# Optimization experiments

Measured on AMD Instinct MI355X. Metric: run time of the kernel, lower is better.

The kernel has to match this reference:

```python
import jax, jax.numpy as jnp
import numpy as np
from jax import lax

S, B, T, H, V = 128, 32, 64, 512, 32000
H2 = 2 * H


def setup_inputs() -> dict:
    key = jax.random.key(0)
    ks = jax.random.split(key, 12)
    sc = 0.02  # small init scale to keep softmax/log numerically tame
    return {
        "h_s": jax.random.normal(ks[0], (S, B, H2), jnp.float32),
        "s_mask": jnp.ones((S, B, 1), jnp.float32),
        "w_a": jax.random.normal(ks[1], (H2, H), jnp.float32) * sc,
        "v_a": jax.random.normal(ks[2], (H, H), jnp.float32) * sc,
        "u_a": jax.random.normal(ks[3], (H, 1), jnp.float32) * sc,
        "w_b": jax.random.normal(ks[4], (H, V), jnp.float32) * sc,
        "v_b": jax.random.normal(ks[5], (H2, V), jnp.float32) * sc,
        "W_ih": jax.random.normal(ks[6], (4 * H, H2), jnp.float32) * sc,
        "W_hh": jax.random.normal(ks[7], (4 * H, H), jnp.float32) * sc,
        "b_ih": jnp.zeros((4 * H,), jnp.float32),
        "b_hh": jnp.zeros((4 * H,), jnp.float32),
        "t_mask": jnp.ones((T, B), jnp.float32),
        "t_indices": jax.random.randint(ks[8], (T, B), 0, V, jnp.int32),
    }


def reference(h_s, s_mask, w_a, v_a, u_a, w_b, v_b, W_ih, W_hh, b_ih, b_hh, t_mask, t_indices):
    # h_s: [S,B,2H] encoder states, s_mask: [S,B,1]
    wa_h = h_s @ w_a  # precompute w_a(h_i) once (same math as per-step recompute): [S,B,H]
    b = b_ih + b_hh
    Tn = t_indices.shape[0]

    def step(carry, _):
        s, c = carry  # s = LSTM hidden state, c = cell state, each [B,H]
        # Bahdanau additive attention (original multiplies logits by mask, then softmax)
        scores = jnp.tanh(wa_h + s @ v_a) @ u_a          # [S,B,1]
        alpha = jax.nn.softmax(scores * s_mask, axis=0)   # [S,B,1]
        ct = jnp.sum(alpha * h_s, axis=0)                 # [B,2H]
        # torch LSTMCell: gates order i,f,g,o
        gates = ct @ W_ih.T + s @ W_hh.T + b              # [B,4H]
        i, f, g, o = jnp.split(gates, 4, axis=1)
        c_new = jax.nn.sigmoid(f) * c + jax.nn.sigmoid(i) * jnp.tanh(g)
        s_new = jax.nn.sigmoid(o) * jnp.tanh(c_new)
        p = jax.nn.softmax(s_new @ w_b + ct @ v_b, axis=1)  # [B,V]
        return (s_new, c_new), p

    nb = h_s.shape[1]
    init = (jnp.zeros((nb, H), h_s.dtype), jnp.zeros((nb, H), h_s.dtype))
    _, p_gen = lax.scan(step, init, None, length=Tn)      # [T,B,V]

    # masked mean NLL per batch element
    probs = jnp.take_along_axis(p_gen, t_indices[:, :, None], axis=2)[..., 0]  # [T,B]
    nll = -jnp.log(probs) * t_mask
    loss = jnp.sum(nll, axis=0) / jnp.sum(t_mask, axis=0)  # [B]
    return loss, p_gen
```

## Files before the change

### kernel.cpp

```cpp
#include <hip/hip_runtime.h>

typedef __attribute__((ext_vector_type(8))) short bf16x8;
typedef __attribute__((ext_vector_type(4))) float f32x4;
typedef __attribute__((ext_vector_type(4))) unsigned int u32x4;

#define NWG_ 256

__device__ __forceinline__ unsigned short f2b(float x){
  union { float f; unsigned u; } v; v.f = x;
  unsigned r = v.u + 0x7FFFu + ((v.u >> 16) & 1u);
  return (unsigned short)(r >> 16);
}
__device__ __forceinline__ float b2f(unsigned short h){
  union { float f; unsigned u; } v; v.u = ((unsigned)h) << 16; return v.f;
}
__device__ __forceinline__ float rcpf_(float x){ return __builtin_amdgcn_rcpf(x); }
__device__ __forceinline__ float tanhf_(float x){
  x = fminf(15.f, fmaxf(-15.f, x));
  float e = __expf(2.f*x);
  return (e - 1.f) * rcpf_(e + 1.f);
}
__device__ __forceinline__ float sigf_(float x){
  x = fminf(30.f, fmaxf(-30.f, x));
  return rcpf_(1.f + __expf(-x));
}

__global__ void k_convert(const float* __restrict__ h_s, const float* __restrict__ w_a,
                          const float* __restrict__ W_ih, const float* __restrict__ v_a,
                          const float* __restrict__ W_hh, const float* __restrict__ b_ih,
                          const float* __restrict__ b_hh,
                          unsigned short* __restrict__ hs_b, unsigned short* __restrict__ Wcomb,
                          unsigned short* __restrict__ Wv, unsigned short* __restrict__ Whh_p,
                          float* __restrict__ bias_p)
{
  const int total = 4194304 + 524288 + 2097152 + 262144 + 1048576 + 2048;
  for (int i = blockIdx.x*256 + threadIdx.x; i < total; i += gridDim.x*256) {
    int j = i;
    if (j < 4194304) { hs_b[j] = f2b(h_s[j]); continue; }
    j -= 4194304;
    if (j < 524288) { int k = j >> 9, n = j & 511;
      Wcomb[n*1024 + k] = f2b(w_a[k*512 + n]); continue; }
    j -= 524288;
    if (j < 2097152) { int rp = j >> 10, k = j & 1023;
      int h = rp >> 2, g = rp & 3;
      Wcomb[(512 + rp)*1024 + k] = f2b(W_ih[(g*512 + h)*1024 + k]); continue; }
    j -= 2097152;
    if (j < 262144) { int k = j >> 9, h = j & 511;
      Wv[h*512 + k] = f2b(v_a[k*512 + h]); continue; }
    j -= 262144;
    if (j < 1048576) { int rp = j >> 9, k = j & 511;
      int h = rp >> 2, g = rp & 3;
      Whh_p[rp*512 + k] = f2b(W_hh[(g*512 + h)*512 + k]); continue; }
    j -= 1048576;
    { int rp = j; int h = rp >> 2, g = rp & 3;
      bias_p[rp] = b_ih[g*512 + h] + b_hh[g*512 + h]; }
  }
}

__global__ __launch_bounds__(256) void k_convB(const float* __restrict__ w_b,
                                               const float* __restrict__ v_b,
                                               unsigned short* __restrict__ Bt)
{
  __shared__ unsigned short T[64*80];
  const int k0 = blockIdx.x*64, n0 = blockIdx.y*64;
  const int tx = threadIdx.x;
  const int kk = tx >> 4, nn = (tx & 15)*4;
  #pragma unroll
  for (int i = 0; i < 4; ++i) {
    int kr = k0 + kk + i*16;
    const float* src = (kr < 512) ? &w_b[(size_t)kr*32000 + n0 + nn]
                                  : &v_b[(size_t)(kr-512)*32000 + n0 + nn];
    f32x4 v = *(const f32x4*)src;
    T[(nn+0)*80 + kk + i*16] = f2b(v.x);
    T[(nn+1)*80 + kk + i*16] = f2b(v.y);
    T[(nn+2)*80 + kk + i*16] = f2b(v.z);
    T[(nn+3)*80 + kk + i*16] = f2b(v.w);
  }
  __syncthreads();
  #pragma unroll
  for (int i = 0; i < 2; ++i) {
    int p = tx + i*256;
    int nrow = p >> 3, kp = p & 7;
    *(u32x4*)&Bt[(size_t)(n0+nrow)*1536 + k0 + kp*8] = *(const u32x4*)&T[nrow*80 + kp*8];
  }
}

#define BM 128
#define BN 128
#define BK 64
#define LDT 72

__global__ __launch_bounds__(256) void k_gemm(
  const unsigned short* __restrict__ A,
  const float* __restrict__ B0, const float* __restrict__ B1, int bsplit,
  const unsigned short* __restrict__ Bnk, int mode,
  void* __restrict__ C0, void* __restrict__ C1, int ncut, int ldc0, int ldc1, int cbf,
  float* __restrict__ Zp,
  int M, int N, int K)
{
  __shared__ unsigned short As[BM*LDT];
  __shared__ unsigned short Bs[BN*LDT];
  const int tx = threadIdx.x;
  const int m0 = blockIdx.x * BM, n0 = blockIdx.y * BN;
  const int wave = tx >> 6, lane = tx & 63;
  const int wm = (wave >> 1) * 64, wn = (wave & 1) * 64;
  const int q = lane >> 4, r16 = lane & 15;
  f32x4 acc[4][4];
  #pragma unroll
  for (int i=0;i<4;i++)
    #pragma unroll
    for (int j=0;j<4;j++) acc[i][j] = (f32x4){0.f,0.f,0.f,0.f};

  for (int k0 = 0; k0 < K; k0 += BK) {
    #pragma unroll
    for (int i = 0; i < 4; ++i) {
      int idx = tx + i*256;
      int row = idx >> 3, piece = idx & 7;
      *(u32x4*)&As[row*LDT + piece*8] =
        *(const u32x4*)&A[(size_t)(m0+row)*K + k0 + piece*8];
    }
    if (mode == 0) {
      #pragma unroll
      for (int i = 0; i < 8; ++i) {
        int idx = tx + i*256;
        int kk = idx >> 5, nn = (idx & 31)*4;
        int kg = k0 + kk;
        const float* src = (kg < bsplit) ? (B0 + (size_t)kg*N) : (B1 + (size_t)(kg - bsplit)*N);
        f32x4 v = *(const f32x4*)&src[n0 + nn];
        Bs[(nn+0)*LDT + kk] = f2b(v.x);
        Bs[(nn+1)*LDT + kk] = f2b(v.y);
        Bs[(nn+2)*LDT + kk] = f2b(v.z);
        Bs[(nn+3)*LDT + kk] = f2b(v.w);
      }
    } else {
      #pragma unroll
      for (int i = 0; i < 4; ++i) {
        int idx = tx + i*256;
        int row = idx >> 3, piece = idx & 7;
        *(u32x4*)&Bs[row*LDT + piece*8] =
          *(const u32x4*)&Bnk[(size_t)(n0+row)*K + k0 + piece*8];
      }
    }
    __syncthreads();
    #pragma unroll
    for (int kk = 0; kk < BK; kk += 32) {
      bf16x8 af[4], bfv[4];
      #pragma unroll
      for (int i=0;i<4;i++) af[i] = *(const bf16x8*)&As[(wm + i*16 + r16)*LDT + kk + q*8];
      #pragma unroll
      for (int j=0;j<4;j++) bfv[j] = *(const bf16x8*)&Bs[(wn + j*16 + r16)*LDT + kk + q*8];
      #pragma unroll
      for (int i=0;i<4;i++)
        #pragma unroll
        for (int j=0;j<4;j++)
          acc[i][j] = __builtin_amdgcn_mfma_f32_16x16x32_bf16(af[i], bfv[j], acc[i][j], 0,0,0);
    }
    __syncthreads();
  }
  if (Zp) {
    #pragma unroll
    for (int i=0;i<4;i++)
      #pragma unroll
      for (int reg=0; reg<4; ++reg) {
        float z = __expf(acc[i][0][reg]) + __expf(acc[i][1][reg])
                + __expf(acc[i][2][reg]) + __expf(acc[i][3][reg]);
        z += __shfl_xor(z, 1, 64); z += __shfl_xor(z, 2, 64);
        z += __shfl_xor(z, 4, 64); z += __shfl_xor(z, 8, 64);
        if (r16 == 0) atomicAdd(&Zp[m0 + wm + i*16 + q*4 + reg], z);
      }
  }
  #pragma unroll
  for (int i=0;i<4;i++)
    #pragma unroll
    for (int j=0;j<4;j++) {
      int n = n0 + wn + j*16 + r16;
      #pragma unroll
      for (int reg=0; reg<4; ++reg) {
        int m = m0 + wm + i*16 + q*4 + reg;
        float v = acc[i][j][reg];
        if (n < ncut) {
          if (cbf) ((unsigned short*)C0)[(size_t)m*ldc0 + n] = f2b(v);
          else     ((float*)C0)[(size_t)m*ldc0 + n] = v;
        } else {
          if (cbf) ((unsigned short*)C1)[(size_t)m*ldc1 + (n-ncut)] = f2b(v);
          else     ((float*)C1)[(size_t)m*ldc1 + (n-ncut)] = v;
        }
      }
    }
}

__device__ __forceinline__ void gbar(unsigned* bar, int w, int* dead) {
  __syncthreads();
  if (*dead) return;
  if (threadIdx.x == 0) {
    unsigned* gen = bar + 288;
    unsigned g = __hip_atomic_load(gen, __ATOMIC_RELAXED, __HIP_MEMORY_SCOPE_AGENT);
    unsigned a = __hip_atomic_fetch_add(&bar[(w & 7)*32], 1u, __ATOMIC_ACQ_REL, __HIP_MEMORY_SCOPE_AGENT);
    bool flipped = false;
    if (a == 31u) {
      unsigned b = __hip_atomic_fetch_add(bar + 256, 1u, __ATOMIC_ACQ_REL, __HIP_MEMORY_SCOPE_AGENT);
      if (b == 7u) {
        #pragma unroll
        for (int i = 0; i < 8; ++i)
          __hip_atomic_store(&bar[i*32], 0u, __ATOMIC_RELAXED, __HIP_MEMORY_SCOPE_AGENT);
        __hip_atomic_store(bar + 256, 0u, __ATOMIC_RELAXED, __HIP_MEMORY_SCOPE_AGENT);
        __hip_atomic_store(gen, g + 1u, __ATOMIC_RELEASE, __HIP_MEMORY_SCOPE_AGENT);
        flipped = true;
      }
    }
    if (!flipped) {
      long sp = 0;
      while (__hip_atomic_load(gen, __ATOMIC_RELAXED, __HIP_MEMORY_SCOPE_AGENT) == g) {
        __builtin_amdgcn_s_sleep(8);
        if (++sp > 400000L) { *dead = 1; break; }
      }
    }
    __builtin_amdgcn_fence(__ATOMIC_ACQUIRE, "agent");
  }
  __syncthreads();
}

__global__ __launch_bounds__(256) void k_recur(
  const unsigned short* __restrict__ wa_h,
  const unsigned short* __restrict__ G,
  const unsigned short* __restrict__ hs_b,
  const unsigned short* __restrict__ Wv,
  const unsigned short* __restrict__ Whh_p,
  const float* __restrict__ bias_p,
  const float* __restrict__ s_mask,
  const float* __restrict__ u_a,
  float* __restrict__ c_st,
  float* __restrict__ sva_g,
  float* __restrict__ whh_g,
  float* __restrict__ scores_g,
  unsigned short* __restrict__ Abf,
  unsigned* bar)
{
  __shared__ float AL[128];
  __shared__ float GL[256];
  __shared__ float RD[2048];
  __shared__ int s_dead;
  const int w = blockIdx.x, tx = threadIdx.x;
  if (tx == 0) s_dead = 0;
  { int gid = w*256 + tx; if (gid < 32*512) c_st[gid] = 0.f; }
  gbar(bar, w, &s_dead);

  const int wave = tx >> 6, lane = tx & 63;
  const f32x4 ua0 = *(const f32x4*)&u_a[lane*8];
  const f32x4 ua1 = *(const f32x4*)&u_a[lane*8 + 4];

  for (int t = 0; t < 64; ++t) {
    if (w < 160) {
      if (t == 0) {
        for (int o = tx; o < 512; o += 256) {
          int b = o >> 4, rl = o & 15;
          int nc = w*16 + rl;
          if (nc < 512) sva_g[b*512 + nc] = 0.f;
          else          whh_g[b*2048 + (nc - 512)] = 0.f;
        }
      } else {
        const int q = lane >> 4, rl = lane & 15;
        const int ncol = w*16 + rl;
        const unsigned short* bp = (ncol < 512) ? (Wv + (size_t)ncol*512)
                                                : (Whh_p + (size_t)(ncol-512)*512);
        f32x4 a0 = (f32x4){0.f,0.f,0.f,0.f}, a1 = (f32x4){0.f,0.f,0.f,0.f};
        const size_t arow0 = ((size_t)(t-1)*32 + rl) * 1536;
        const size_t arow1 = ((size_t)(t-1)*32 + 16 + rl) * 1536;
        #pragma unroll
        for (int ks = 0; ks < 4; ++ks) {
          int kg = (wave*4 + ks)*32 + q*8;
          bf16x8 fa0 = *(const bf16x8*)&Abf[arow0 + kg];
          bf16x8 fa1 = *(const bf16x8*)&Abf[arow1 + kg];
          bf16x8 fb  = *(const bf16x8*)&bp[kg];
          a0 = __builtin_amdgcn_mfma_f32_16x16x32_bf16(fa0, fb, a0, 0,0,0);
          a1 = __builtin_amdgcn_mfma_f32_16x16x32_bf16(fa1, fb, a1, 0,0,0);
        }
        #pragma unroll
        for (int reg = 0; reg < 4; ++reg) {
          RD[(wave*32 + (q*4 + reg))*16 + rl]      = a0[reg];
          RD[(wave*32 + (16 + q*4 + reg))*16 + rl] = a1[reg];
        }
        __syncthreads();
        for (int o = tx; o < 512; o += 256) {
          int b = o >> 4, rlo = o & 15;
          float v = RD[(b)*16 + rlo] + RD[(32 + b)*16 + rlo]
                  + RD[(64 + b)*16 + rlo] + RD[(96 + b)*16 + rlo];
          int nc = w*16 + rlo;
          if (nc < 512) sva_g[b*512 + nc] = v;
          else          whh_g[b*2048 + (nc - 512)] = v;
        }
      }
    }
    gbar(bar, w, &s_dead);

    {
      #pragma unroll
      for (int r = 0; r < 4; ++r) {
        int p = w*16 + wave*4 + r;
        int b = p & 31, s = p >> 5;
        bf16x8 wv8 = *(const bf16x8*)&wa_h[(size_t)p*512 + lane*8];
        const float* sv = &sva_g[b*512 + lane*8];
        f32x4 s0 = *(const f32x4*)sv, s1 = *(const f32x4*)(sv + 4);
        float acc;
        acc  = tanhf_(b2f(wv8[0]) + s0.x) * ua0.x;
        acc += tanhf_(b2f(wv8[1]) + s0.y) * ua0.y;
        acc += tanhf_(b2f(wv8[2]) + s0.z) * ua0.z;
        acc += tanhf_(b2f(wv8[3]) + s0.w) * ua0.w;
        acc += tanhf_(b2f(wv8[4]) + s1.x) * ua1.x;
        acc += tanhf_(b2f(wv8[5]) + s1.y) * ua1.y;
        acc += tanhf_(b2f(wv8[6]) + s1.z) * ua1.z;
        acc += tanhf_(b2f(wv8[7]) + s1.w) * ua1.w;
        #pragma unroll
        for (int o = 32; o > 0; o >>= 1) acc += __shfl_down(acc, o, 64);
        if (lane == 0) scores_g[b*128 + s] = acc * s_mask[s*32 + b];
      }
    }
    gbar(bar, w, &s_dead);

    {
      const int b = w >> 3, ch = w & 7;
      if (tx < 128) AL[tx] = __expf(scores_g[b*128 + tx]);
      __syncthreads();
      if (tx < 64) {
        float sm = AL[tx] + AL[tx + 64];
        #pragma unroll
        for (int o = 32; o > 0; o >>= 1) sm += __shfl_down(sm, o, 64);
        if (tx == 0) GL[0] = rcpf_(sm);
      }
      __syncthreads();
      float inv = GL[0];
      __syncthreads();
      if (tx < 128) AL[tx] *= inv;
      __syncthreads();
      {
        const int cg = tx & 31, sg = tx >> 5;
        const int nn = ch*256 + cg*8;
        float a8[8] = {0.f,0.f,0.f,0.f,0.f,0.f,0.f,0.f};
        #pragma unroll
        for (int k = 0; k < 16; ++k) {
          int s = sg*16 + k;
          float av = AL[s];
          bf16x8 g8 = *(const bf16x8*)&G[((size_t)s*32 + b)*2048 + nn];
          a8[0] += av * b2f(g8[0]); a8[1] += av * b2f(g8[1]);
          a8[2] += av * b2f(g8[2]); a8[3] += av * b2f(g8[3]);
          a8[4] += av * b2f(g8[4]); a8[5] += av * b2f(g8[5]);
          a8[6] += av * b2f(g8[6]); a8[7] += av * b2f(g8[7]);
        }
        #pragma unroll
        for (int j = 0; j < 8; ++j) RD[(cg*8 + j)*8 + sg] = a8[j];
      }
      __syncthreads();
      {
        int n = ch*256 + tx;
        float sum = 0.f;
        #pragma unroll
        for (int k = 0; k < 8; ++k) sum += RD[tx*8 + k];
        GL[tx] = sum + whh_g[b*2048 + n] + bias_p[n];
      }
      __syncthreads();
      if (tx < 64) {
        int h = ch*64 + tx;
        float iv = GL[tx*4+0], fv = GL[tx*4+1], gv = GL[tx*4+2], ov = GL[tx*4+3];
        float co = c_st[b*512 + h];
        float cn = sigf_(fv)*co + sigf_(iv)*tanhf_(gv);
        float sn = sigf_(ov)*tanhf_(cn);
        c_st[b*512 + h] = cn;
        Abf[((size_t)t*32 + b)*1536 + h] = f2b(sn);
      }
      {
        const int cg2 = tx & 15, sg2 = tx >> 4;
        const int jj = ch*128 + cg2*8;
        float c8[8] = {0.f,0.f,0.f,0.f,0.f,0.f,0.f,0.f};
        #pragma unroll
        for (int k = 0; k < 8; ++k) {
          int s = sg2*8 + k;
          float av = AL[s];
          bf16x8 h8 = *(const bf16x8*)&hs_b[((size_t)s*32 + b)*1024 + jj];
          c8[0] += av * b2f(h8[0]); c8[1] += av * b2f(h8[1]);
          c8[2] += av * b2f(h8[2]); c8[3] += av * b2f(h8[3]);
          c8[4] += av * b2f(h8[4]); c8[5] += av * b2f(h8[5]);
          c8[6] += av * b2f(h8[6]); c8[7] += av * b2f(h8[7]);
        }
        __syncthreads();
        #pragma unroll
        for (int j = 0; j < 8; ++j) RD[(cg2*8 + j)*16 + sg2] = c8[j];
      }
      __syncthreads();
      if (tx < 128) {
        float sum = 0.f;
        #pragma unroll
        for (int k = 0; k < 16; ++k) sum += RD[tx*16 + k];
        Abf[((size_t)t*32 + b)*1536 + 512 + ch*128 + tx] = f2b(sum);
      }
    }
    gbar(bar, w, &s_dead);
  }
}

__global__ __launch_bounds__(64) void k_loss(const float* __restrict__ L, const float* __restrict__ Z,
                                             const int* __restrict__ t_idx, const float* __restrict__ t_mask,
                                             float* __restrict__ out)
{
  const int b = blockIdx.x, t = threadIdx.x;
  const int row = t*32 + b;
  int id = t_idx[t*32 + b];
  float m = t_mask[t*32 + b];
  float l = L[(size_t)row*32000 + id];
  float v = (__logf(Z[row]) - l) * m;
  float vm = v, mm = m;
  for (int o = 32; o > 0; o >>= 1) { vm += __shfl_down(vm, o, 64); mm += __shfl_down(mm, o, 64); }
  if (t == 0) out[b] = vm / mm;
}

__global__ __launch_bounds__(256) void k_s2(float* __restrict__ L, const float* __restrict__ Z)
{
  const int row = blockIdx.x, tx = threadIdx.x;
  float* p = L + (size_t)row*32000;
  float rz = 1.f / Z[row];
  for (int n = tx; n < 32000; n += 256) p[n] = __expf(p[n]) * rz;
}

extern "C" void kernel_launch(void* const* d_in, const int* in_sizes, int n_in,
                              void* d_out, int out_size, void* d_ws, size_t ws_size,
                              hipStream_t stream)
{
  (void)in_sizes; (void)n_in; (void)out_size;
  const float* h_s    = (const float*)d_in[0];
  const float* s_mask = (const float*)d_in[1];
  const float* w_a    = (const float*)d_in[2];
  const float* v_a    = (const float*)d_in[3];
  const float* u_a    = (const float*)d_in[4];
  const float* w_b    = (const float*)d_in[5];
  const float* v_b    = (const float*)d_in[6];
  const float* W_ih   = (const float*)d_in[7];
  const float* W_hh   = (const float*)d_in[8];
  const float* b_ih   = (const float*)d_in[9];
  const float* b_hh   = (const float*)d_in[10];
  const float* t_mask = (const float*)d_in[11];
  const int*   t_idx  = (const int*)d_in[12];
  float* out = (float*)d_out;
  float* logits = out + 32;

  char* w = (char*)d_ws;
  size_t off = 0;
  auto take = [&](size_t bytes) -> void* {
    void* p = w + off; off += (bytes + 255) & ~(size_t)255; return p;
  };
  unsigned* bar          = (unsigned*)take(2048);
  float* c_st            = (float*)take((size_t)32*512*4);
  float* sva_g           = (float*)take((size_t)32*512*4);
  float* whh_g           = (float*)take((size_t)32*2048*4);
  float* scores_g        = (float*)take((size_t)32*128*4);
  float* Z               = (float*)take((size_t)2048*4);
  float* bias_p          = (float*)take((size_t)2048*4);
  unsigned short* hs_b   = (unsigned short*)take((size_t)4096*1024*2);
  unsigned short* Wcomb  = (unsigned short*)take((size_t)2560*1024*2);
  unsigned short* Wv     = (unsigned short*)take((size_t)512*512*2);
  unsigned short* Whh_p  = (unsigned short*)take((size_t)2048*512*2);
  unsigned short* wa_hb  = (unsigned short*)take((size_t)4096*512*2);
  unsigned short* G      = (unsigned short*)take((size_t)4096*2048*2);
  unsigned short* Abf    = (unsigned short*)take((size_t)2048*1536*2);
  size_t base_need = off;
  bool useBt = (ws_size >= base_need + (size_t)32000*1536*2 + 256);
  unsigned short* Bt = useBt ? (unsigned short*)take((size_t)32000*1536*2) : nullptr;

  hipMemsetAsync(bar, 0, 2048, stream);
  hipMemsetAsync(Z, 0, 2048*4, stream);
  k_convert<<<4096, 256, 0, stream>>>(h_s, w_a, W_ih, v_a, W_hh, b_ih, b_hh,
                                      hs_b, Wcomb, Wv, Whh_p, bias_p);
  if (useBt)
    k_convB<<<dim3(24, 500), 256, 0, stream>>>(w_b, v_b, Bt);
  k_gemm<<<dim3(32,20), 256, 0, stream>>>(hs_b, nullptr, nullptr, 0, Wcomb, 1,
                                          wa_hb, G, 512, 512, 2048, 1, nullptr,
                                          4096, 2560, 1024);
  k_recur<<<NWG_, 256, 0, stream>>>(wa_hb, G, hs_b, Wv, Whh_p, bias_p, s_mask, u_a,
                                    c_st, sva_g, whh_g, scores_g, Abf, bar);
  if (useBt)
    k_gemm<<<dim3(16,250), 256, 0, stream>>>(Abf, nullptr, nullptr, 0, Bt, 1,
                                             logits, logits, 32000, 32000, 32000, 0, Z,
                                             2048, 32000, 1536);
  else
    k_gemm<<<dim3(16,250), 256, 0, stream>>>(Abf, w_b, v_b, 512, nullptr, 0,
                                             logits, logits, 32000, 32000, 32000, 0, Z,
                                             2048, 32000, 1536);
  k_loss<<<32, 64, 0, stream>>>(logits, Z, t_idx, t_mask, out);
  k_s2<<<2048, 256, 0, stream>>>(logits, Z);
}
```

Baseline: 3.015 ms.

## Replace grid-wide barriers with per-batch group barriers in recurrent kernel

The recurrent kernel now partitions work so each batch element is owned by a group of 8 workgroups, which synchronise through per-batch phase slots instead of a grid-wide 256-block barrier. The hidden-state matvecs (s@v_a and s@W_hh) are computed locally per group with scalar dot products, rather than by MFMA across 160 blocks reading Abf. Cell state and the W_hh projection are kept in shared memory, and softmax normalisation is deferred into the reductions. This cuts grid-wide synchronisation latency in exchange for more redundant weight reads per group and non-MFMA matvecs.

```diff
diff --git a/kernel.cpp b/kernel.cpp
--- a/kernel.cpp
+++ b/kernel.cpp
@@ -4,7 +4,8 @@
 typedef __attribute__((ext_vector_type(4))) float f32x4;
 typedef __attribute__((ext_vector_type(4))) unsigned int u32x4;
 
-#define NWG_ 256
+#define AG  __HIP_MEMORY_SCOPE_AGENT
+#define RLX __ATOMIC_RELAXED
 
 __device__ __forceinline__ unsigned short f2b(float x){
   union { float f; unsigned u; } v; v.f = x;
@@ -189,35 +190,34 @@
     }
 }
 
-__device__ __forceinline__ void gbar(unsigned* bar, int w, int* dead) {
+__device__ __forceinline__ void group_bar(unsigned* slots, int ch, int wv, int lane,
+                                          unsigned ph, volatile int* dead)
+{
   __syncthreads();
-  if (*dead) return;
-  if (threadIdx.x == 0) {
-    unsigned* gen = bar + 288;
-    unsigned g = __hip_atomic_load(gen, __ATOMIC_RELAXED, __HIP_MEMORY_SCOPE_AGENT);
-    unsigned a = __hip_atomic_fetch_add(&bar[(w & 7)*32], 1u, __ATOMIC_ACQ_REL, __HIP_MEMORY_SCOPE_AGENT);
-    bool flipped = false;
-    if (a == 31u) {
-      unsigned b = __hip_atomic_fetch_add(bar + 256, 1u, __ATOMIC_ACQ_REL, __HIP_MEMORY_SCOPE_AGENT);
-      if (b == 7u) {
-        #pragma unroll
-        for (int i = 0; i < 8; ++i)
-          __hip_atomic_store(&bar[i*32], 0u, __ATOMIC_RELAXED, __HIP_MEMORY_SCOPE_AGENT);
-        __hip_atomic_store(bar + 256, 0u, __ATOMIC_RELAXED, __HIP_MEMORY_SCOPE_AGENT);
-        __hip_atomic_store(gen, g + 1u, __ATOMIC_RELEASE, __HIP_MEMORY_SCOPE_AGENT);
-        flipped = true;
-      }
-    }
-    if (!flipped) {
-      long sp = 0;
-      while (__hip_atomic_load(gen, __ATOMIC_RELAXED, __HIP_MEMORY_SCOPE_AGENT) == g) {
-        __builtin_amdgcn_s_sleep(8);
-        if (++sp > 400000L) { *dead = 1; break; }
-      }
-    }
-    __builtin_amdgcn_fence(__ATOMIC_ACQUIRE, "agent");
+  if (wv == 0 && !*dead) {
+    if (lane == 0)
+      __hip_atomic_store(&slots[ch], ph, RLX, AG);
+    long sp = 0;
+    for (;;) {
+      unsigned v = __hip_atomic_load(&slots[lane & 7], RLX, AG);
+      if (__all((int)(v >= ph))) break;
+      __builtin_amdgcn_s_sleep(2);
+      if (++sp > 1500000L) { *dead = 1; break; }
+    }
   }
   __syncthreads();
+}
+
+__device__ __forceinline__ float dot8_(bf16x8 w8, const float* sp) {
+  float a0 =      b2f((unsigned short)w8[0]) * sp[0];
+  float a1 =      b2f((unsigned short)w8[1]) * sp[1];
+  a0 = fmaf(b2f((unsigned short)w8[2]), sp[2], a0);
+  a1 = fmaf(b2f((unsigned short)w8[3]), sp[3], a1);
+  a0 = fmaf(b2f((unsigned short)w8[4]), sp[4], a0);
+  a1 = fmaf(b2f((unsigned short)w8[5]), sp[5], a1);
+  a0 = fmaf(b2f((unsigned short)w8[6]), sp[6], a0);
+  a1 = fmaf(b2f((unsigned short)w8[7]), sp[7], a1);
+  return a0 + a1;
 }
 
 __global__ __launch_bounds__(256) void k_recur(
@@ -229,171 +229,164 @@
   const float* __restrict__ bias_p,
   const float* __restrict__ s_mask,
   const float* __restrict__ u_a,
-  float* __restrict__ c_st,
-  float* __restrict__ sva_g,
-  float* __restrict__ whh_g,
-  float* __restrict__ scores_g,
+  float* __restrict__ s_comm,
+  float* __restrict__ sva_comm,
+  float* __restrict__ scores_comm,
   unsigned short* __restrict__ Abf,
-  unsigned* bar)
-{
+  unsigned* __restrict__ bar)
+{
+  __shared__ float s_sh[512];
+  __shared__ float sva_sh[512];
+  __shared__ float whh_sh[256];
   __shared__ float AL[128];
   __shared__ float GL[256];
   __shared__ float RD[2048];
+  __shared__ float c_sh[64];
+  __shared__ float invs;
   __shared__ int s_dead;
+
   const int w = blockIdx.x, tx = threadIdx.x;
+  const int b = w >> 3, ch = w & 7;
+  const int wv = tx >> 6, lane = tx & 63;
+  unsigned* slots = bar + b*64;
+
   if (tx == 0) s_dead = 0;
-  { int gid = w*256 + tx; if (gid < 32*512) c_st[gid] = 0.f; }
-  gbar(bar, w, &s_dead);
-
-  const int wave = tx >> 6, lane = tx & 63;
+  if (tx < 64) c_sh[tx] = 0.f;
+  if (tx < 64)
+    __hip_atomic_store(&s_comm[b*512 + ch*64 + tx], 0.f, RLX, AG);
+
   const f32x4 ua0 = *(const f32x4*)&u_a[lane*8];
   const f32x4 ua1 = *(const f32x4*)&u_a[lane*8 + 4];
 
+  group_bar(slots, ch, wv, lane, 1u, &s_dead);
+
   for (int t = 0; t < 64; ++t) {
-    if (w < 160) {
-      if (t == 0) {
-        for (int o = tx; o < 512; o += 256) {
-          int b = o >> 4, rl = o & 15;
-          int nc = w*16 + rl;
-          if (nc < 512) sva_g[b*512 + nc] = 0.f;
-          else          whh_g[b*2048 + (nc - 512)] = 0.f;
-        }
-      } else {
-        const int q = lane >> 4, rl = lane & 15;
-        const int ncol = w*16 + rl;
-        const unsigned short* bp = (ncol < 512) ? (Wv + (size_t)ncol*512)
-                                                : (Whh_p + (size_t)(ncol-512)*512);
-        f32x4 a0 = (f32x4){0.f,0.f,0.f,0.f}, a1 = (f32x4){0.f,0.f,0.f,0.f};
-        const size_t arow0 = ((size_t)(t-1)*32 + rl) * 1536;
-        const size_t arow1 = ((size_t)(t-1)*32 + 16 + rl) * 1536;
-        #pragma unroll
-        for (int ks = 0; ks < 4; ++ks) {
-          int kg = (wave*4 + ks)*32 + q*8;
-          bf16x8 fa0 = *(const bf16x8*)&Abf[arow0 + kg];
-          bf16x8 fa1 = *(const bf16x8*)&Abf[arow1 + kg];
-          bf16x8 fb  = *(const bf16x8*)&bp[kg];
-          a0 = __builtin_amdgcn_mfma_f32_16x16x32_bf16(fa0, fb, a0, 0,0,0);
-          a1 = __builtin_amdgcn_mfma_f32_16x16x32_bf16(fa1, fb, a1, 0,0,0);
-        }
-        #pragma unroll
-        for (int reg = 0; reg < 4; ++reg) {
-          RD[(wave*32 + (q*4 + reg))*16 + rl]      = a0[reg];
-          RD[(wave*32 + (16 + q*4 + reg))*16 + rl] = a1[reg];
-        }
-        __syncthreads();
-        for (int o = tx; o < 512; o += 256) {
-          int b = o >> 4, rlo = o & 15;
-          float v = RD[(b)*16 + rlo] + RD[(32 + b)*16 + rlo]
-                  + RD[(64 + b)*16 + rlo] + RD[(96 + b)*16 + rlo];
-          int nc = w*16 + rlo;
-          if (nc < 512) sva_g[b*512 + nc] = v;
-          else          whh_g[b*2048 + (nc - 512)] = v;
-        }
-      }
-    }
-    gbar(bar, w, &s_dead);
-
+    const unsigned ph0 = 2u + 3u*(unsigned)t;
+
+    for (int i = tx; i < 512; i += 256)
+      s_sh[i] = __hip_atomic_load(&s_comm[b*512 + i], RLX, AG);
+    __syncthreads();
     {
-      #pragma unroll
-      for (int r = 0; r < 4; ++r) {
-        int p = w*16 + wave*4 + r;
-        int b = p & 31, s = p >> 5;
-        bf16x8 wv8 = *(const bf16x8*)&wa_h[(size_t)p*512 + lane*8];
-        const float* sv = &sva_g[b*512 + lane*8];
-        f32x4 s0 = *(const f32x4*)sv, s1 = *(const f32x4*)(sv + 4);
-        float acc;
-        acc  = tanhf_(b2f(wv8[0]) + s0.x) * ua0.x;
-        acc += tanhf_(b2f(wv8[1]) + s0.y) * ua0.y;
-        acc += tanhf_(b2f(wv8[2]) + s0.z) * ua0.z;
-        acc += tanhf_(b2f(wv8[3]) + s0.w) * ua0.w;
-        acc += tanhf_(b2f(wv8[4]) + s1.x) * ua1.x;
-        acc += tanhf_(b2f(wv8[5]) + s1.y) * ua1.y;
-        acc += tanhf_(b2f(wv8[6]) + s1.z) * ua1.z;
-        acc += tanhf_(b2f(wv8[7]) + s1.w) * ua1.w;
+      const float* sp = &s_sh[lane*8];
+      const unsigned short* __restrict__ wvb = Wv + (size_t)(ch*64)*512;
+      #pragma unroll 4
+      for (int r = wv; r < 64; r += 4) {
+        bf16x8 w8 = *(const bf16x8*)&wvb[(size_t)r*512 + lane*8];
+        float acc = dot8_(w8, sp);
         #pragma unroll
         for (int o = 32; o > 0; o >>= 1) acc += __shfl_down(acc, o, 64);
-        if (lane == 0) scores_g[b*128 + s] = acc * s_mask[s*32 + b];
-      }
-    }
-    gbar(bar, w, &s_dead);
-
+        if (lane == 0)
+          __hip_atomic_store(&sva_comm[b*512 + ch*64 + r], acc, RLX, AG);
+      }
+      const unsigned short* __restrict__ whb = Whh_p + (size_t)(ch*256)*512;
+      #pragma unroll 4
+      for (int r = wv; r < 256; r += 4) {
+        bf16x8 w8 = *(const bf16x8*)&whb[(size_t)r*512 + lane*8];
+        float acc = dot8_(w8, sp);
+        #pragma unroll
+        for (int o = 32; o > 0; o >>= 1) acc += __shfl_down(acc, o, 64);
+        if (lane == 0) whh_sh[r] = acc;
+      }
+    }
+    group_bar(slots, ch, wv, lane, ph0, &s_dead);
+
+    for (int i = tx; i < 512; i += 256)
+      sva_sh[i] = __hip_atomic_load(&sva_comm[b*512 + i], RLX, AG);
+    __syncthreads();
     {
-      const int b = w >> 3, ch = w & 7;
-      if (tx < 128) AL[tx] = __expf(scores_g[b*128 + tx]);
+      const float* sp = &sva_sh[lane*8];
+      #pragma unroll
+      for (int si = 0; si < 4; ++si) {
+        const int s = ch*16 + wv*4 + si;
+        bf16x8 w8 = *(const bf16x8*)&wa_h[((size_t)s*32 + b)*512 + lane*8];
+        float acc;
+        acc  = tanhf_(b2f((unsigned short)w8[0]) + sp[0]) * ua0.x;
+        acc += tanhf_(b2f((unsigned short)w8[1]) + sp[1]) * ua0.y;
+        acc += tanhf_(b2f((unsigned short)w8[2]) + sp[2]) * ua0.z;
+        acc += tanhf_(b2f((unsigned short)w8[3]) + sp[3]) * ua0.w;
+        acc += tanhf_(b2f((unsigned short)w8[4]) + sp[4]) * ua1.x;
+        acc += tanhf_(b2f((unsigned short)w8[5]) + sp[5]) * ua1.y;
+        acc += tanhf_(b2f((unsigned short)w8[6]) + sp[6]) * ua1.z;
+        acc += tanhf_(b2f((unsigned short)w8[7]) + sp[7]) * ua1.w;
+        #pragma unroll
+        for (int o = 32; o > 0; o >>= 1) acc += __shfl_down(acc, o, 64);
+        if (lane == 0)
+          __hip_atomic_store(&scores_comm[b*128 + s], acc * s_mask[s*32 + b], RLX, AG);
+      }
+    }
+    group_bar(slots, ch, wv, lane, ph0 + 1u, &s_dead);
+
+    if (tx < 128)
+      AL[tx] = __expf(__hip_atomic_load(&scores_comm[b*128 + tx], RLX, AG));
+    __syncthreads();
+    if (tx < 64) {
+      float sm = AL[tx] + AL[tx + 64];
+      #pragma unroll
+      for (int o = 32; o > 0; o >>= 1) sm += __shfl_down(sm, o, 64);
+      if (tx == 0) invs = rcpf_(sm);
+    }
+    __syncthreads();
+    {
+      const int cg = tx & 31, sg = tx >> 5;
+      const int nn = ch*256 + cg*8;
+      float a8[8] = {0.f,0.f,0.f,0.f,0.f,0.f,0.f,0.f};
+      #pragma unroll
+      for (int k = 0; k < 16; ++k) {
+        int s = sg*16 + k;
+        float av = AL[s];
+        bf16x8 g8 = *(const bf16x8*)&G[((size_t)s*32 + b)*2048 + nn];
+        a8[0] += av * b2f((unsigned short)g8[0]); a8[1] += av * b2f((unsigned short)g8[1]);
+        a8[2] += av * b2f((unsigned short)g8[2]); a8[3] += av * b2f((unsigned short)g8[3]);
+        a8[4] += av * b2f((unsigned short)g8[4]); a8[5] += av * b2f((unsigned short)g8[5]);
+        a8[6] += av * b2f((unsigned short)g8[6]); a8[7] += av * b2f((unsigned short)g8[7]);
+      }
+      #pragma unroll
+      for (int j = 0; j < 8; ++j) RD[(cg*8 + j)*8 + sg] = a8[j];
+    }
+    __syncthreads();
+    {
+      float sum = 0.f;
+      #pragma unroll
+      for (int k = 0; k < 8; ++k) sum += RD[tx*8 + k];
+      GL[tx] = sum * invs + whh_sh[tx] + bias_p[ch*256 + tx];
+    }
+    __syncthreads();
+    if (tx < 64) {
+      float iv = GL[tx*4+0], fv = GL[tx*4+1], gv = GL[tx*4+2], ov = GL[tx*4+3];
+      float co = c_sh[tx];
+      float cn = sigf_(fv)*co + sigf_(iv)*tanhf_(gv);
+      float sn = sigf_(ov)*tanhf_(cn);
+      c_sh[tx] = cn;
+      __hip_atomic_store(&s_comm[b*512 + ch*64 + tx], sn, RLX, AG);
+      Abf[((size_t)t*32 + b)*1536 + ch*64 + tx] = f2b(sn);
+    }
+    {
+      const int cg2 = tx & 15, sg2 = tx >> 4;
+      const int jj = ch*128 + cg2*8;
+      float c8[8] = {0.f,0.f,0.f,0.f,0.f,0.f,0.f,0.f};
+      #pragma unroll
+      for (int k = 0; k < 8; ++k) {
+        int s = sg2*8 + k;
+        float av = AL[s];
+        bf16x8 h8 = *(const bf16x8*)&hs_b[((size_t)s*32 + b)*1024 + jj];
+        c8[0] += av * b2f((unsigned short)h8[0]); c8[1] += av * b2f((unsigned short)h8[1]);
+        c8[2] += av * b2f((unsigned short)h8[2]); c8[3] += av * b2f((unsigned short)h8[3]);
+        c8[4] += av * b2f((unsigned short)h8[4]); c8[5] += av * b2f((unsigned short)h8[5]);
+        c8[6] += av * b2f((unsigned short)h8[6]); c8[7] += av * b2f((unsigned short)h8[7]);
+      }
       __syncthreads();
-      if (tx < 64) {
-        float sm = AL[tx] + AL[tx + 64];
-        #pragma unroll
-        for (int o = 32; o > 0; o >>= 1) sm += __shfl_down(sm, o, 64);
-        if (tx == 0) GL[0] = rcpf_(sm);
-      }
-      __syncthreads();
-      float inv = GL[0];
-      __syncthreads();
-      if (tx < 128) AL[tx] *= inv;
-      __syncthreads();
-      {
-        const int cg = tx & 31, sg = tx >> 5;
-        const int nn = ch*256 + cg*8;
-        float a8[8] = {0.f,0.f,0.f,0.f,0.f,0.f,0.f,0.f};
-        #pragma unroll
-        for (int k = 0; k < 16; ++k) {
-          int s = sg*16 + k;
-          float av = AL[s];
-          bf16x8 g8 = *(const bf16x8*)&G[((size_t)s*32 + b)*2048 + nn];
-          a8[0] += av * b2f(g8[0]); a8[1] += av * b2f(g8[1]);
-          a8[2] += av * b2f(g8[2]); a8[3] += av * b2f(g8[3]);
-          a8[4] += av * b2f(g8[4]); a8[5] += av * b2f(g8[5]);
-          a8[6] += av * b2f(g8[6]); a8[7] += av * b2f(g8[7]);
-        }
-        #pragma unroll
-        for (int j = 0; j < 8; ++j) RD[(cg*8 + j)*8 + sg] = a8[j];
-      }
-      __syncthreads();
-      {
-        int n = ch*256 + tx;
-        float sum = 0.f;
-        #pragma unroll
-        for (int k = 0; k < 8; ++k) sum += RD[tx*8 + k];
-        GL[tx] = sum + whh_g[b*2048 + n] + bias_p[n];
-      }
-      __syncthreads();
-      if (tx < 64) {
-        int h = ch*64 + tx;
-        float iv = GL[tx*4+0], fv = GL[tx*4+1], gv = GL[tx*4+2], ov = GL[tx*4+3];
-        float co = c_st[b*512 + h];
-        float cn = sigf_(fv)*co + sigf_(iv)*tanhf_(gv);
-        float sn = sigf_(ov)*tanhf_(cn);
-        c_st[b*512 + h] = cn;
-        Abf[((size_t)t*32 + b)*1536 + h] = f2b(sn);
-      }
-      {
-        const int cg2 = tx & 15, sg2 = tx >> 4;
-        const int jj = ch*128 + cg2*8;
-        float c8[8] = {0.f,0.f,0.f,0.f,0.f,0.f,0.f,0.f};
-        #pragma unroll
-        for (int k = 0; k < 8; ++k) {
-          int s = sg2*8 + k;
-          float av = AL[s];
-          bf16x8 h8 = *(const bf16x8*)&hs_b[((size_t)s*32 + b)*1024 + jj];
-          c8[0] += av * b2f(h8[0]); c8[1] += av * b2f(h8[1]);
-          c8[2] += av * b2f(h8[2]); c8[3] += av * b2f(h8[3]);
-          c8[4] += av * b2f(h8[4]); c8[5] += av * b2f(h8[5]);
-          c8[6] += av * b2f(h8[6]); c8[7] += av * b2f(h8[7]);
-        }
-        __syncthreads();
-        #pragma unroll
-        for (int j = 0; j < 8; ++j) RD[(cg2*8 + j)*16 + sg2] = c8[j];
-      }
-      __syncthreads();
-      if (tx < 128) {
-        float sum = 0.f;
-        #pragma unroll
-        for (int k = 0; k < 16; ++k) sum += RD[tx*16 + k];
-        Abf[((size_t)t*32 + b)*1536 + 512 + ch*128 + tx] = f2b(sum);
-      }
-    }
-    gbar(bar, w, &s_dead);
+      #pragma unroll
+      for (int j = 0; j < 8; ++j) RD[(cg2*8 + j)*16 + sg2] = c8[j];
+    }
+    __syncthreads();
+    if (tx < 128) {
+      float sum = 0.f;
+      #pragma unroll
+      for (int k = 0; k < 16; ++k) sum += RD[tx*16 + k];
+      Abf[((size_t)t*32 + b)*1536 + 512 + ch*128 + tx] = f2b(sum * invs);
+    }
+    if (t < 63)
+      group_bar(slots, ch, wv, lane, ph0 + 2u, &s_dead);
   }
 }
 
@@ -446,11 +439,10 @@
   auto take = [&](size_t bytes) -> void* {
     void* p = w + off; off += (bytes + 255) & ~(size_t)255; return p;
   };
-  unsigned* bar          = (unsigned*)take(2048);
-  float* c_st            = (float*)take((size_t)32*512*4);
-  float* sva_g           = (float*)take((size_t)32*512*4);
-  float* whh_g           = (float*)take((size_t)32*2048*4);
-  float* scores_g        = (float*)take((size_t)32*128*4);
+  unsigned* bar          = (unsigned*)take((size_t)32*64*4);
+  float* s_comm          = (float*)take((size_t)32*512*4);
+  float* sva_comm        = (float*)take((size_t)32*512*4);
+  float* scores_comm     = (float*)take((size_t)32*128*4);
   float* Z               = (float*)take((size_t)2048*4);
   float* bias_p          = (float*)take((size_t)2048*4);
   unsigned short* hs_b   = (unsigned short*)take((size_t)4096*1024*2);
@@ -464,7 +456,7 @@
   bool useBt = (ws_size >= base_need + (size_t)32000*1536*2 + 256);
   unsigned short* Bt = useBt ? (unsigned short*)take((size_t)32000*1536*2) : nullptr;
 
-  hipMemsetAsync(bar, 0, 2048, stream);
+  hipMemsetAsync(bar, 0, (size_t)32*64*4, stream);
   hipMemsetAsync(Z, 0, 2048*4, stream);
   k_convert<<<4096, 256, 0, stream>>>(h_s, w_a, W_ih, v_a, W_hh, b_ih, b_hh,
                                       hs_b, Wcomb, Wv, Whh_p, bias_p);
@@ -473,8 +465,8 @@
   k_gemm<<<dim3(32,20), 256, 0, stream>>>(hs_b, nullptr, nullptr, 0, Wcomb, 1,
                                           wa_hb, G, 512, 512, 2048, 1, nullptr,
                                           4096, 2560, 1024);
-  k_recur<<<NWG_, 256, 0, stream>>>(wa_hb, G, hs_b, Wv, Whh_p, bias_p, s_mask, u_a,
-                                    c_st, sva_g, whh_g, scores_g, Abf, bar);
+  k_recur<<<256, 256, 0, stream>>>(wa_hb, G, hs_b, Wv, Whh_p, bias_p, s_mask, u_a,
+                                   s_comm, sva_comm, scores_comm, Abf, bar);
   if (useBt)
     k_gemm<<<dim3(16,250), 256, 0, stream>>>(Abf, nullptr, nullptr, 0, Bt, 1,
                                              logits, logits, 32000, 32000, 32000, 0, Z,
```

After: 4.229 ms. +40.3%, slower.

## Use monotonic-phase grid barrier and keep LSTM state on-chip in recurrence

Applied to the files above, without the earlier changes.

Replaces the generation-counter grid barrier, which reset its counters every round, with a monotonic phase-counting barrier that has 16 sub-counters and uses relaxed atomics plus an explicit vmcnt wait. The initial barrier and the barrier after the final step are dropped. Cell state now lives in LDS per workgroup, and the hidden state is published as packed bf16 through a small buffer that is staged into LDS before the matvec. Cross-workgroup data is read and written with agent-scope atomics so that caches do not return stale values. This cuts barrier latency and global traffic per step, but correctness now relies on relaxed-ordering memory semantics.

```diff
diff --git a/kernel.cpp b/kernel.cpp
--- a/kernel.cpp
+++ b/kernel.cpp
@@ -4,7 +4,8 @@
 typedef __attribute__((ext_vector_type(4))) float f32x4;
 typedef __attribute__((ext_vector_type(4))) unsigned int u32x4;
 
-#define NWG_ 256
+#define AG  __HIP_MEMORY_SCOPE_AGENT
+#define RLX __ATOMIC_RELAXED
 
 __device__ __forceinline__ unsigned short f2b(float x){
   union { float f; unsigned u; } v; v.f = x;
@@ -189,33 +190,23 @@
     }
 }
 
-__device__ __forceinline__ void gbar(unsigned* bar, int w, int* dead) {
+__device__ __forceinline__ void gbar(unsigned* bar, int w, unsigned ph, volatile int* dead) {
   __syncthreads();
   if (*dead) return;
   if (threadIdx.x == 0) {
-    unsigned* gen = bar + 288;
-    unsigned g = __hip_atomic_load(gen, __ATOMIC_RELAXED, __HIP_MEMORY_SCOPE_AGENT);
-    unsigned a = __hip_atomic_fetch_add(&bar[(w & 7)*32], 1u, __ATOMIC_ACQ_REL, __HIP_MEMORY_SCOPE_AGENT);
-    bool flipped = false;
-    if (a == 31u) {
-      unsigned b = __hip_atomic_fetch_add(bar + 256, 1u, __ATOMIC_ACQ_REL, __HIP_MEMORY_SCOPE_AGENT);
-      if (b == 7u) {
-        #pragma unroll
-        for (int i = 0; i < 8; ++i)
-          __hip_atomic_store(&bar[i*32], 0u, __ATOMIC_RELAXED, __HIP_MEMORY_SCOPE_AGENT);
-        __hip_atomic_store(bar + 256, 0u, __ATOMIC_RELAXED, __HIP_MEMORY_SCOPE_AGENT);
-        __hip_atomic_store(gen, g + 1u, __ATOMIC_RELEASE, __HIP_MEMORY_SCOPE_AGENT);
-        flipped = true;
-      }
-    }
-    if (!flipped) {
-      long sp = 0;
-      while (__hip_atomic_load(gen, __ATOMIC_RELAXED, __HIP_MEMORY_SCOPE_AGENT) == g) {
-        __builtin_amdgcn_s_sleep(8);
-        if (++sp > 400000L) { *dead = 1; break; }
-      }
-    }
-    __builtin_amdgcn_fence(__ATOMIC_ACQUIRE, "agent");
+    asm volatile("s_waitcnt vmcnt(0)" ::: "memory");
+    unsigned* gen = bar + 520;
+    unsigned a = __hip_atomic_fetch_add(&bar[(w & 15)*32], 1u, RLX, AG);
+    if (a == ph*16u - 1u) {
+      unsigned m = __hip_atomic_fetch_add(bar + 512, 1u, RLX, AG);
+      if (m == ph*16u - 1u)
+        __hip_atomic_store(gen, ph, RLX, AG);
+    }
+    long sp = 0;
+    while (__hip_atomic_load(gen, RLX, AG) < ph) {
+      __builtin_amdgcn_s_sleep(4);
+      if (++sp > 3000000L) { *dead = 1; break; }
+    }
   }
   __syncthreads();
 }
@@ -229,69 +220,69 @@
   const float* __restrict__ bias_p,
   const float* __restrict__ s_mask,
   const float* __restrict__ u_a,
-  float* __restrict__ c_st,
   float* __restrict__ sva_g,
   float* __restrict__ whh_g,
   float* __restrict__ scores_g,
+  unsigned* __restrict__ s_bf,
   unsigned short* __restrict__ Abf,
   unsigned* bar)
 {
+  __shared__ unsigned s_lds[32*260];
   __shared__ float AL[128];
   __shared__ float GL[256];
   __shared__ float RD[2048];
+  __shared__ float c_sh[64];
   __shared__ int s_dead;
+
   const int w = blockIdx.x, tx = threadIdx.x;
+  const int wave = tx >> 6, lane = tx & 63;
   if (tx == 0) s_dead = 0;
-  { int gid = w*256 + tx; if (gid < 32*512) c_st[gid] = 0.f; }
-  gbar(bar, w, &s_dead);
-
-  const int wave = tx >> 6, lane = tx & 63;
+  if (tx < 64) c_sh[tx] = 0.f;
+
   const f32x4 ua0 = *(const f32x4*)&u_a[lane*8];
   const f32x4 ua1 = *(const f32x4*)&u_a[lane*8 + 4];
 
   for (int t = 0; t < 64; ++t) {
+    const unsigned ph0 = 1u + 3u*(unsigned)t;
+
     if (w < 160) {
-      if (t == 0) {
-        for (int o = tx; o < 512; o += 256) {
-          int b = o >> 4, rl = o & 15;
-          int nc = w*16 + rl;
-          if (nc < 512) sva_g[b*512 + nc] = 0.f;
-          else          whh_g[b*2048 + (nc - 512)] = 0.f;
-        }
-      } else {
-        const int q = lane >> 4, rl = lane & 15;
-        const int ncol = w*16 + rl;
-        const unsigned short* bp = (ncol < 512) ? (Wv + (size_t)ncol*512)
-                                                : (Whh_p + (size_t)(ncol-512)*512);
-        f32x4 a0 = (f32x4){0.f,0.f,0.f,0.f}, a1 = (f32x4){0.f,0.f,0.f,0.f};
-        const size_t arow0 = ((size_t)(t-1)*32 + rl) * 1536;
-        const size_t arow1 = ((size_t)(t-1)*32 + 16 + rl) * 1536;
-        #pragma unroll
-        for (int ks = 0; ks < 4; ++ks) {
-          int kg = (wave*4 + ks)*32 + q*8;
-          bf16x8 fa0 = *(const bf16x8*)&Abf[arow0 + kg];
-          bf16x8 fa1 = *(const bf16x8*)&Abf[arow1 + kg];
-          bf16x8 fb  = *(const bf16x8*)&bp[kg];
-          a0 = __builtin_amdgcn_mfma_f32_16x16x32_bf16(fa0, fb, a0, 0,0,0);
-          a1 = __builtin_amdgcn_mfma_f32_16x16x32_bf16(fa1, fb, a1, 0,0,0);
-        }
-        #pragma unroll
-        for (int reg = 0; reg < 4; ++reg) {
-          RD[(wave*32 + (q*4 + reg))*16 + rl]      = a0[reg];
-          RD[(wave*32 + (16 + q*4 + reg))*16 + rl] = a1[reg];
-        }
-        __syncthreads();
-        for (int o = tx; o < 512; o += 256) {
-          int b = o >> 4, rlo = o & 15;
-          float v = RD[(b)*16 + rlo] + RD[(32 + b)*16 + rlo]
-                  + RD[(64 + b)*16 + rlo] + RD[(96 + b)*16 + rlo];
-          int nc = w*16 + rlo;
-          if (nc < 512) sva_g[b*512 + nc] = v;
-          else          whh_g[b*2048 + (nc - 512)] = v;
-        }
-      }
-    }
-    gbar(bar, w, &s_dead);
+      #pragma unroll 8
+      for (int i = tx; i < 32*256; i += 256) {
+        unsigned v = __hip_atomic_load(&s_bf[i], RLX, AG);
+        s_lds[(i >> 8)*260 + (i & 255)] = v;
+      }
+      __syncthreads();
+      const int q = lane >> 4, rl = lane & 15;
+      const int ncol = w*16 + rl;
+      const unsigned short* bp = (ncol < 512) ? (Wv + (size_t)ncol*512)
+                                              : (Whh_p + (size_t)(ncol-512)*512);
+      f32x4 a0 = (f32x4){0.f,0.f,0.f,0.f}, a1 = (f32x4){0.f,0.f,0.f,0.f};
+      #pragma unroll
+      for (int ks = 0; ks < 4; ++ks) {
+        int kg = (wave*4 + ks)*32 + q*8;
+        int ku = (wave*4 + ks)*16 + q*4;
+        bf16x8 fa0 = *(const bf16x8*)&s_lds[rl*260 + ku];
+        bf16x8 fa1 = *(const bf16x8*)&s_lds[(16 + rl)*260 + ku];
+        bf16x8 fb  = *(const bf16x8*)&bp[kg];
+        a0 = __builtin_amdgcn_mfma_f32_16x16x32_bf16(fa0, fb, a0, 0,0,0);
+        a1 = __builtin_amdgcn_mfma_f32_16x16x32_bf16(fa1, fb, a1, 0,0,0);
+      }
+      #pragma unroll
+      for (int reg = 0; reg < 4; ++reg) {
+        RD[(wave*32 + (q*4 + reg))*16 + rl]      = a0[reg];
+        RD[(wave*32 + (16 + q*4 + reg))*16 + rl] = a1[reg];
+      }
+      __syncthreads();
+      for (int o = tx; o < 512; o += 256) {
+        int bq = o >> 4, rlo = o & 15;
+        float v = RD[bq*16 + rlo] + RD[(32 + bq)*16 + rlo]
+                + RD[(64 + bq)*16 + rlo] + RD[(96 + bq)*16 + rlo];
+        int nc = w*16 + rlo;
+        if (nc < 512) __hip_atomic_store(&sva_g[bq*512 + nc], v, RLX, AG);
+        else          __hip_atomic_store(&whh_g[bq*2048 + (nc - 512)], v, RLX, AG);
+      }
+    }
+    gbar(bar, w, ph0, &s_dead);
 
     {
       #pragma unroll
@@ -299,27 +290,31 @@
         int p = w*16 + wave*4 + r;
         int b = p & 31, s = p >> 5;
         bf16x8 wv8 = *(const bf16x8*)&wa_h[(size_t)p*512 + lane*8];
-        const float* sv = &sva_g[b*512 + lane*8];
-        f32x4 s0 = *(const f32x4*)sv, s1 = *(const f32x4*)(sv + 4);
+        float sv[8];
+        #pragma unroll
+        for (int j = 0; j < 8; ++j)
+          sv[j] = __hip_atomic_load(&sva_g[b*512 + lane*8 + j], RLX, AG);
         float acc;
-        acc  = tanhf_(b2f(wv8[0]) + s0.x) * ua0.x;
-        acc += tanhf_(b2f(wv8[1]) + s0.y) * ua0.y;
-        acc += tanhf_(b2f(wv8[2]) + s0.z) * ua0.z;
-        acc += tanhf_(b2f(wv8[3]) + s0.w) * ua0.w;
-        acc += tanhf_(b2f(wv8[4]) + s1.x) * ua1.x;
-        acc += tanhf_(b2f(wv8[5]) + s1.y) * ua1.y;
-        acc += tanhf_(b2f(wv8[6]) + s1.z) * ua1.z;
-        acc += tanhf_(b2f(wv8[7]) + s1.w) * ua1.w;
+        acc  = tanhf_(b2f((unsigned short)wv8[0]) + sv[0]) * ua0.x;
+        acc += tanhf_(b2f((unsigned short)wv8[1]) + sv[1]) * ua0.y;
+        acc += tanhf_(b2f((unsigned short)wv8[2]) + sv[2]) * ua0.z;
+        acc += tanhf_(b2f((unsigned short)wv8[3]) + sv[3]) * ua0.w;
+        acc += tanhf_(b2f((unsigned short)wv8[4]) + sv[4]) * ua1.x;
+        acc += tanhf_(b2f((unsigned short)wv8[5]) + sv[5]) * ua1.y;
+        acc += tanhf_(b2f((unsigned short)wv8[6]) + sv[6]) * ua1.z;
+        acc += tanhf_(b2f((unsigned short)wv8[7]) + sv[7]) * ua1.w;
         #pragma unroll
         for (int o = 32; o > 0; o >>= 1) acc += __shfl_down(acc, o, 64);
-        if (lane == 0) scores_g[b*128 + s] = acc * s_mask[s*32 + b];
-      }
-    }
-    gbar(bar, w, &s_dead);
+        if (lane == 0)
+          __hip_atomic_store(&scores_g[b*128 + s], acc * s_mask[s*32 + b], RLX, AG);
+      }
+    }
+    gbar(bar, w, ph0 + 1u, &s_dead);
 
     {
       const int b = w >> 3, ch = w & 7;
-      if (tx < 128) AL[tx] = __expf(scores_g[b*128 + tx]);
+      if (tx < 128)
+        AL[tx] = __expf(__hip_atomic_load(&scores_g[b*128 + tx], RLX, AG));
       __syncthreads();
       if (tx < 64) {
         float sm = AL[tx] + AL[tx + 64];
@@ -341,10 +336,10 @@
           int s = sg*16 + k;
           float av = AL[s];
           bf16x8 g8 = *(const bf16x8*)&G[((size_t)s*32 + b)*2048 + nn];
-          a8[0] += av * b2f(g8[0]); a8[1] += av * b2f(g8[1]);
-          a8[2] += av * b2f(g8[2]); a8[3] += av * b2f(g8[3]);
-          a8[4] += av * b2f(g8[4]); a8[5] += av * b2f(g8[5]);
-          a8[6] += av * b2f(g8[6]); a8[7] += av * b2f(g8[7]);
+          a8[0] += av * b2f((unsigned short)g8[0]); a8[1] += av * b2f((unsigned short)g8[1]);
+          a8[2] += av * b2f((unsigned short)g8[2]); a8[3] += av * b2f((unsigned short)g8[3]);
+          a8[4] += av * b2f((unsigned short)g8[4]); a8[5] += av * b2f((unsigned short)g8[5]);
+          a8[6] += av * b2f((unsigned short)g8[6]); a8[7] += av * b2f((unsigned short)g8[7]);
         }
         #pragma unroll
         for (int j = 0; j < 8; ++j) RD[(cg*8 + j)*8 + sg] = a8[j];
@@ -355,17 +350,23 @@
         float sum = 0.f;
         #pragma unroll
         for (int k = 0; k < 8; ++k) sum += RD[tx*8 + k];
-        GL[tx] = sum + whh_g[b*2048 + n] + bias_p[n];
+        GL[tx] = sum + __hip_atomic_load(&whh_g[b*2048 + n], RLX, AG) + bias_p[n];
       }
       __syncthreads();
       if (tx < 64) {
-        int h = ch*64 + tx;
         float iv = GL[tx*4+0], fv = GL[tx*4+1], gv = GL[tx*4+2], ov = GL[tx*4+3];
-        float co = c_st[b*512 + h];
+        float co = c_sh[tx];
         float cn = sigf_(fv)*co + sigf_(iv)*tanhf_(gv);
         float sn = sigf_(ov)*tanhf_(cn);
-        c_st[b*512 + h] = cn;
-        Abf[((size_t)t*32 + b)*1536 + h] = f2b(sn);
+        c_sh[tx] = cn;
+        int h = ch*64 + tx;
+        unsigned short hb = f2b(sn);
+        Abf[((size_t)t*32 + b)*1536 + h] = hb;
+        unsigned nb = (unsigned)__shfl_down((int)hb, 1, 64);
+        if ((tx & 1) == 0) {
+          unsigned pk = (unsigned)hb | (nb << 16);
+          __hip_atomic_store(&s_bf[b*256 + (h >> 1)], pk, RLX, AG);
+        }
       }
       {
         const int cg2 = tx & 15, sg2 = tx >> 4;
@@ -376,10 +377,10 @@
           int s = sg2*8 + k;
           float av = AL[s];
           bf16x8 h8 = *(const bf16x8*)&hs_b[((size_t)s*32 + b)*1024 + jj];
-          c8[0] += av * b2f(h8[0]); c8[1] += av * b2f(h8[1]);
-          c8[2] += av * b2f(h8[2]); c8[3] += av * b2f(h8[3]);
-          c8[4] += av * b2f(h8[4]); c8[5] += av * b2f(h8[5]);
-          c8[6] += av * b2f(h8[6]); c8[7] += av * b2f(h8[7]);
+          c8[0] += av * b2f((unsigned short)h8[0]); c8[1] += av * b2f((unsigned short)h8[1]);
+          c8[2] += av * b2f((unsigned short)h8[2]); c8[3] += av * b2f((unsigned short)h8[3]);
+          c8[4] += av * b2f((unsigned short)h8[4]); c8[5] += av * b2f((unsigned short)h8[5]);
+          c8[6] += av * b2f((unsigned short)h8[6]); c8[7] += av * b2f((unsigned short)h8[7]);
         }
         __syncthreads();
         #pragma unroll
@@ -393,7 +394,8 @@
         Abf[((size_t)t*32 + b)*1536 + 512 + ch*128 + tx] = f2b(sum);
       }
     }
-    gbar(bar, w, &s_dead);
+    if (t < 63)
+      gbar(bar, w, ph0 + 2u, &s_dead);
   }
 }
 
@@ -446,11 +448,11 @@
   auto take = [&](size_t bytes) -> void* {
     void* p = w + off; off += (bytes + 255) & ~(size_t)255; return p;
   };
-  unsigned* bar          = (unsigned*)take(2048);
-  float* c_st            = (float*)take((size_t)32*512*4);
+  unsigned* bar          = (unsigned*)take(4096);
   float* sva_g           = (float*)take((size_t)32*512*4);
   float* whh_g           = (float*)take((size_t)32*2048*4);
   float* scores_g        = (float*)take((size_t)32*128*4);
+  unsigned* s_bf         = (unsigned*)take((size_t)32*256*4);
   float* Z               = (float*)take((size_t)2048*4);
   float* bias_p          = (float*)take((size_t)2048*4);
   unsigned short* hs_b   = (unsigned short*)take((size_t)4096*1024*2);
@@ -464,7 +466,8 @@
   bool useBt = (ws_size >= base_need + (size_t)32000*1536*2 + 256);
   unsigned short* Bt = useBt ? (unsigned short*)take((size_t)32000*1536*2) : nullptr;
 
-  hipMemsetAsync(bar, 0, 2048, stream);
+  hipMemsetAsync(bar, 0, 4096, stream);
+  hipMemsetAsync(s_bf, 0, (size_t)32*256*4, stream);
   hipMemsetAsync(Z, 0, 2048*4, stream);
   k_convert<<<4096, 256, 0, stream>>>(h_s, w_a, W_ih, v_a, W_hh, b_ih, b_hh,
                                       hs_b, Wcomb, Wv, Whh_p, bias_p);
@@ -473,8 +476,8 @@
   k_gemm<<<dim3(32,20), 256, 0, stream>>>(hs_b, nullptr, nullptr, 0, Wcomb, 1,
                                           wa_hb, G, 512, 512, 2048, 1, nullptr,
                                           4096, 2560, 1024);
-  k_recur<<<NWG_, 256, 0, stream>>>(wa_hb, G, hs_b, Wv, Whh_p, bias_p, s_mask, u_a,
-                                    c_st, sva_g, whh_g, scores_g, Abf, bar);
+  k_recur<<<256, 256, 0, stream>>>(wa_hb, G, hs_b, Wv, Whh_p, bias_p, s_mask, u_a,
+                                   sva_g, whh_g, scores_g, s_bf, Abf, bar);
   if (useBt)
     k_gemm<<<dim3(16,250), 256, 0, stream>>>(Abf, nullptr, nullptr, 0, Bt, 1,
                                              logits, logits, 32000, 32000, 32000, 0, Z,
```

After: 3.051 ms. About the same (+1.2%).
